# Kernel tuning notes

Measured on AMD Instinct MI355X. Metric: run time of the kernel, lower is better.

The kernel has to match this reference:

```python
import jax, jax.numpy as jnp
import numpy as np

S, D, N, O = 8192, 64, 2048, 8  # samples(paths), input_dim, nodes per hidden layer, output_dim
T = 1.0  # temperature for every layer (temperatures = [1,1,1,1])


def setup_inputs() -> dict:
    key = jax.random.key(0)
    ks = jax.random.split(key, 9)
    return {
        "x": jax.random.normal(ks[0], (S, D), dtype=jnp.float32),
        "w0": jax.random.normal(ks[1], (N, D), dtype=jnp.float32),
        "w1": jax.random.normal(ks[2], (N, N), dtype=jnp.float32),
        "w2": jax.random.normal(ks[3], (N, N), dtype=jnp.float32),
        "w_out": jax.random.normal(ks[4], (O, N), dtype=jnp.float32),
        # pre-drawn categorical keys, one per (sample, node) per layer, as in get_proba
        "c0": jax.random.randint(ks[5], (S, N), 0, D, dtype=jnp.int32),
        "c1": jax.random.randint(ks[6], (S, N), 0, N, dtype=jnp.int32),
        "c2": jax.random.randint(ks[7], (S, N), 0, N, dtype=jnp.int32),
        "keys_out": jax.random.randint(ks[8], (S, O), 0, N, dtype=jnp.int32),
    }


def reference(x, w0, w1, w2, w_out, c0, c1, c2, keys_out):
    # routing log-probabilities: log softmax(W / T) over inputs (dim=1)
    lp0 = jax.nn.log_softmax(w0 / T, axis=1)      # [N, D]
    lp1 = jax.nn.log_softmax(w1 / T, axis=1)      # [N, N]
    lp2 = jax.nn.log_softmax(w2 / T, axis=1)      # [N, N]
    lp_out = jax.nn.log_softmax(w_out / T, axis=1)  # [O, N]

    s_idx = jnp.arange(S)[:, None]                # [S, 1]
    o_idx = jnp.arange(O)[None, :]                # [1, O]

    # walk the sampled path backwards from each output node, accumulating log-prob
    r2 = keys_out                                  # [S, O] node chosen in hidden layer 2
    logp = lp_out[o_idx, r2]
    r1 = c2[s_idx, r2]                             # [S, O] node chosen in hidden layer 1
    logp = logp + lp2[r2, r1]
    r0 = c1[s_idx, r1]                             # [S, O] node chosen in hidden layer 0
    logp = logp + lp1[r1, r0]
    cin = c0[s_idx, r0]                            # [S, O] input feature selected
    logp = logp + lp0[r0, cin]

    probas = jnp.exp(logp)                         # [S, O] path probabilities (get_proba)
    # arity-1 base function sin at every node: y = sin(sin(sin(x[s, cin])))
    y = jnp.sin(jnp.sin(jnp.sin(x[s_idx, cin])))   # [S, O] forward path evaluation
    return jnp.stack([y, probas])                  # [2, S, O]
```

## Files before the change

kernel.cpp:

```cpp
#include <hip/hip_runtime.h>
#include <math.h>
#include <float.h>

#define S 8192
#define D 64
#define N 2048
#define O 8

__global__ __launch_bounds__(256) void lse_all_kernel(
    const float* __restrict__ w0, const float* __restrict__ w1,
    const float* __restrict__ w2, const float* __restrict__ w_out,
    float* __restrict__ ws) {
    int b = blockIdx.x;
    const float* w;
    int W, row;
    float* out;
    if (b < N)          { w = w0;    W = D; row = b;         out = ws;         }
    else if (b < 2 * N) { w = w1;    W = N; row = b - N;     out = ws + N;     }
    else if (b < 3 * N) { w = w2;    W = N; row = b - 2 * N; out = ws + 2 * N; }
    else                { w = w_out; W = N; row = b - 3 * N; out = ws + 3 * N; }

    const float4* rp4 = (const float4*)(w + (size_t)row * W);
    int n4 = W >> 2;

    float m = -FLT_MAX;
    float sum = 0.0f;
    for (int i = threadIdx.x; i < n4; i += 256) {
        float4 v = rp4[i];
        float mv = fmaxf(fmaxf(v.x, v.y), fmaxf(v.z, v.w));
        float nm = fmaxf(m, mv);
        sum = sum * __expf(m - nm)
            + __expf(v.x - nm) + __expf(v.y - nm)
            + __expf(v.z - nm) + __expf(v.w - nm);
        m = nm;
    }

    for (int off = 32; off >= 1; off >>= 1) {
        float mo = __shfl_down(m, off, 64);
        float so = __shfl_down(sum, off, 64);
        float nm = fmaxf(m, mo);
        sum = sum * __expf(m - nm) + so * __expf(mo - nm);
        m = nm;
    }

    __shared__ float sm[4], ss[4];
    int wave = threadIdx.x >> 6;
    int lane = threadIdx.x & 63;
    if (lane == 0) { sm[wave] = m; ss[wave] = sum; }
    __syncthreads();
    if (threadIdx.x == 0) {
        float M = sm[0], Sm = ss[0];
        for (int i = 1; i < 4; ++i) {
            float nm = fmaxf(M, sm[i]);
            Sm = Sm * __expf(M - nm) + ss[i] * __expf(sm[i] - nm);
            M = nm;
        }
        out[row] = M + __logf(Sm);
    }
}

__global__ __launch_bounds__(256) void path_gather_kernel(
    const float* __restrict__ x,
    const float* __restrict__ w0, const float* __restrict__ w1,
    const float* __restrict__ w2, const float* __restrict__ w_out,
    const int* __restrict__ c0, const int* __restrict__ c1,
    const int* __restrict__ c2, const int* __restrict__ keys_out,
    const float* __restrict__ ws, float* __restrict__ out) {
    int t = blockIdx.x * blockDim.x + threadIdx.x;
    int s = t >> 3;
    int o = t & 7;

    const float* lse0 = ws;
    const float* lse1 = ws + N;
    const float* lse2 = ws + 2 * N;
    const float* lseo = ws + 3 * N;

    int r2 = keys_out[t];
    float logp = w_out[o * N + r2] - lseo[o];

    int r1 = c2[(size_t)s * N + r2];
    logp += w2[(size_t)r2 * N + r1] - lse2[r2];

    int r0 = c1[(size_t)s * N + r1];
    logp += w1[(size_t)r1 * N + r0] - lse1[r1];

    int cin = c0[(size_t)s * N + r0];
    logp += w0[r0 * D + cin] - lse0[r0];

    float y = sinf(sinf(sinf(x[s * D + cin])));

    out[t] = y;
    out[S * O + t] = __expf(logp);
}

extern "C" void kernel_launch(void* const* d_in, const int* in_sizes, int n_in,
                              void* d_out, int out_size, void* d_ws, size_t ws_size,
                              hipStream_t stream) {
    const float* x      = (const float*)d_in[0];
    const float* w0     = (const float*)d_in[1];
    const float* w1     = (const float*)d_in[2];
    const float* w2     = (const float*)d_in[3];
    const float* w_out  = (const float*)d_in[4];
    const int*   c0     = (const int*)d_in[5];
    const int*   c1     = (const int*)d_in[6];
    const int*   c2     = (const int*)d_in[7];
    const int*   keys_o = (const int*)d_in[8];
    float* out = (float*)d_out;
    float* ws  = (float*)d_ws;

    lse_all_kernel<<<3 * N + O, 256, 0, stream>>>(w0, w1, w2, w_out, ws);

    path_gather_kernel<<<(S * O) / 256, 256, 0, stream>>>(
        x, w0, w1, w2, w_out, c0, c1, c2, keys_o, ws, out);
}
```

Measured before the change: 195.7 us.

## Compute one log-sum-exp row per wavefront instead of per block

Reworks the row log-sum-exp kernel so each 64-lane wavefront handles a whole row instead of each 256-thread block. For the 2048-wide rows every lane loads eight float4 values up front, takes one max and then one sum of exponentials, and reduces across the wave with xor shuffles. This removes the shared-memory stage and __syncthreads and cuts the block count by about four. Rows of w0 (64 wide) map one element per lane. In exchange each wave holds more registers and does less latency hiding within a row.

```diff
diff --git a/kernel.cpp b/kernel.cpp
--- a/kernel.cpp
+++ b/kernel.cpp
@@ -11,52 +11,52 @@
     const float* __restrict__ w0, const float* __restrict__ w1,
     const float* __restrict__ w2, const float* __restrict__ w_out,
     float* __restrict__ ws) {
+    int wave = threadIdx.x >> 6;
+    int lane = threadIdx.x & 63;
     int b = blockIdx.x;
-    const float* w;
-    int W, row;
+
+    float m, sum;
     float* out;
-    if (b < N)          { w = w0;    W = D; row = b;         out = ws;         }
-    else if (b < 2 * N) { w = w1;    W = N; row = b - N;     out = ws + N;     }
-    else if (b < 3 * N) { w = w2;    W = N; row = b - 2 * N; out = ws + 2 * N; }
-    else                { w = w_out; W = N; row = b - 3 * N; out = ws + 3 * N; }
+    int row;
 
-    const float4* rp4 = (const float4*)(w + (size_t)row * W);
-    int n4 = W >> 2;
+    if (b < 512) {
+        row = b * 4 + wave;
+        m = w0[row * D + lane];
+        sum = 1.0f;
+        out = ws;
+    } else {
+        int task = (b - 512) * 4 + wave;
+        const float* w;
+        if (task < N)          { w = w1;    row = task;         out = ws + N;     }
+        else if (task < 2 * N) { w = w2;    row = task - N;     out = ws + 2 * N; }
+        else                   { w = w_out; row = task - 2 * N; out = ws + 3 * N; }
 
-    float m = -FLT_MAX;
-    float sum = 0.0f;
-    for (int i = threadIdx.x; i < n4; i += 256) {
-        float4 v = rp4[i];
-        float mv = fmaxf(fmaxf(v.x, v.y), fmaxf(v.z, v.w));
-        float nm = fmaxf(m, mv);
-        sum = sum * __expf(m - nm)
-            + __expf(v.x - nm) + __expf(v.y - nm)
-            + __expf(v.z - nm) + __expf(v.w - nm);
-        m = nm;
+        const float4* rp4 = (const float4*)(w + (size_t)row * N);
+        float4 v[8];
+        #pragma unroll
+        for (int k = 0; k < 8; ++k) v[k] = rp4[lane + 64 * k];
+
+        float mv = -FLT_MAX;
+        #pragma unroll
+        for (int k = 0; k < 8; ++k)
+            mv = fmaxf(mv, fmaxf(fmaxf(v[k].x, v[k].y), fmaxf(v[k].z, v[k].w)));
+        float s = 0.0f;
+        #pragma unroll
+        for (int k = 0; k < 8; ++k)
+            s += __expf(v[k].x - mv) + __expf(v[k].y - mv)
+               + __expf(v[k].z - mv) + __expf(v[k].w - mv);
+        m = mv; sum = s;
     }
 
+    #pragma unroll
     for (int off = 32; off >= 1; off >>= 1) {
-        float mo = __shfl_down(m, off, 64);
-        float so = __shfl_down(sum, off, 64);
+        float mo = __shfl_xor(m, off, 64);
+        float so = __shfl_xor(sum, off, 64);
         float nm = fmaxf(m, mo);
         sum = sum * __expf(m - nm) + so * __expf(mo - nm);
         m = nm;
     }
-
-    __shared__ float sm[4], ss[4];
-    int wave = threadIdx.x >> 6;
-    int lane = threadIdx.x & 63;
-    if (lane == 0) { sm[wave] = m; ss[wave] = sum; }
-    __syncthreads();
-    if (threadIdx.x == 0) {
-        float M = sm[0], Sm = ss[0];
-        for (int i = 1; i < 4; ++i) {
-            float nm = fmaxf(M, sm[i]);
-            Sm = Sm * __expf(M - nm) + ss[i] * __expf(sm[i] - nm);
-            M = nm;
-        }
-        out[row] = M + __logf(Sm);
-    }
+    if (lane == 0) out[row] = m + __logf(sum);
 }
 
 __global__ __launch_bounds__(256) void path_gather_kernel(
@@ -108,7 +108,7 @@
     float* out = (float*)d_out;
     float* ws  = (float*)d_ws;
 
-    lse_all_kernel<<<3 * N + O, 256, 0, stream>>>(w0, w1, w2, w_out, ws);
+    lse_all_kernel<<<512 + (2 * N + O) / 4, 256, 0, stream>>>(w0, w1, w2, w_out, ws);
 
     path_gather_kernel<<<(S * O) / 256, 256, 0, stream>>>(
         x, w0, w1, w2, w_out, c0, c1, c2, keys_o, ws, out);
```

New measurement: 195.2 us. Within noise of the previous version (-0.3%).
